# Optimization experiments

Hardware: AMD Instinct MI355X
Metric: run time of the kernel (lower is better)

## Reference

```python
import jax, jax.numpy as jnp
import numpy as np

B, T, CIN, H, W = 1, 8, 32, 256, 256
CO, NH, WS = 64, 8, 8  # C_out, n_head, wind_size


def conv3x3(x, w, b):
    # x: [N, C, h, w], w: [O, I, 3, 3], stride 1, padding 1 (SAME for 3x3)
    y = jax.lax.conv_general_dilated(
        x, w, window_strides=(1, 1), padding=((1, 1), (1, 1)),
        dimension_numbers=("NCHW", "OIHW", "NCHW"))
    return y + b[None, :, None, None]


def setup_inputs() -> dict:
    key = jax.random.key(0)
    ks = jax.random.split(key, 9)
    s = 0.05  # small init scale keeps attention logits well-conditioned
    f32 = jnp.float32
    return {
        "x": jax.random.normal(ks[0], (B, T, CIN, H, W), f32),
        "Wq": jax.random.normal(ks[1], (CO, CIN, 3, 3), f32) * s,
        "bq": jax.random.normal(ks[2], (CO,), f32) * s,
        "Wk": jax.random.normal(ks[3], (CO, CIN, 3, 3), f32) * s,
        "bk": jax.random.normal(ks[4], (CO,), f32) * s,
        "Wv": jax.random.normal(ks[5], (CO, CIN, 3, 3), f32) * s,
        "bv": jax.random.normal(ks[6], (CO,), f32) * s,
        "Wo": jax.random.normal(ks[7], (CO, CO, 3, 3), f32) * s,
        "bo": jax.random.normal(ks[8], (CO,), f32) * s,
    }


def reference(x, Wq, bq, Wk, bk, Wv, bv, Wo, bo):
    b, t, c, h, w = x.shape
    Hg, Wg = h // WS, w // WS          # grid of windows
    hc = CO // NH                      # per-head channels
    d = hc * WS * WS                   # per-window token dim

    # im2grid: [B,T,C,H,W] -> [B*T*Hg*Wg, C, Ws, Ws] (each window a conv batch elem)
    xg = (x.reshape(b, t, c, Hg, WS, Wg, WS)
           .transpose(0, 1, 3, 5, 2, 4, 6)
           .reshape(b * t * Hg * Wg, c, WS, WS))

    def proj(wgt, bias):
        y = conv3x3(xg, wgt, bias)                        # [BTHWg, CO, Ws, Ws]
        y = y.reshape(b, t, Hg * Wg, NH, hc, WS, WS)      # split heads (nh outer in channel)
        return y.transpose(0, 1, 3, 2, 4, 5, 6).reshape(b, t, NH, Hg * Wg, d)

    q, k, v = proj(Wq, bq), proj(Wk, bk), proj(Wv, bv)    # [B,T,nh,HWg,d]

    att = jnp.einsum("btnqd,btnkd->btnqk", q, k) * (1.0 / np.sqrt(d)).astype(x.dtype)
    att = jax.nn.softmax(att, axis=-1)                    # [B,T,nh,HWg,HWg]
    y = jnp.einsum("btnqk,btnkd->btnqd", att, v)          # [B,T,nh,HWg,d]

    # back to image: [B,T,nh,HWg,hc,Ws,Ws] -> [B,T,CO,Hg,Wg,Ws,Ws] -> [B,T,CO,H,W]
    y = (y.reshape(b, t, NH, Hg * Wg, hc, WS, WS)
          .transpose(0, 1, 2, 4, 3, 5, 6)
          .reshape(b, t, CO, Hg, Wg, WS, WS)
          .transpose(0, 1, 2, 3, 5, 4, 6)
          .reshape(b, t, CO, h, w))

    out = y + conv3x3(y.reshape(b * t, CO, h, w), Wo, bo).reshape(b, t, CO, h, w)
    return out
```

## Files before the change

### kernel.cpp

```cpp
#include <hip/hip_runtime.h>
#include <hip/hip_bf16.h>
#include <stdint.h>


using bf16 = __hip_bfloat16;
typedef short bf16x8 __attribute__((ext_vector_type(8)));
typedef float f32x4 __attribute__((ext_vector_type(4)));

#define AS1 __attribute__((address_space(1)))
#define AS3 __attribute__((address_space(3)))

__device__ __forceinline__ void gload_lds16(const void* g, void* l) {
  __builtin_amdgcn_global_load_lds((const AS1 unsigned int*)g, (AS3 unsigned int*)l, 16, 0, 0);
}
__device__ __forceinline__ float b2f(unsigned short u) {
  union { unsigned int i; float f; } x; x.i = ((unsigned)u) << 16; return x.f;
}
__device__ __forceinline__ unsigned short f2b(float f) {
  __hip_bfloat16 h = __float2bfloat16(f);
  return *reinterpret_cast<unsigned short*>(&h);
}

__global__ __launch_bounds__(256) void prep_w(const float* __restrict__ Wq, const float* __restrict__ Wk,
                                              const float* __restrict__ Wv, const float* __restrict__ Wo,
                                              bf16* __restrict__ wt, bf16* __restrict__ wot) {
  int i = blockIdx.x * 256 + threadIdx.x;
  if (i < 9 * 192 * 32) {
    int ci = i & 31, co192 = (i >> 5) % 192, s = i / 6144;
    int dy = s / 3, dx = s % 3;
    int proj = co192 >> 6, co = co192 & 63;
    const float* Ws = (proj == 0) ? Wq : ((proj == 1) ? Wk : Wv);
    wt[i] = __float2bfloat16(Ws[((co * 32 + ci) * 3 + dy) * 3 + dx]);
  }
  if (i < 9 * 64 * 64) {
    int ci = i & 63, co = (i >> 6) & 63, s = i >> 12;
    wot[i] = __float2bfloat16(Wo[((co * 64 + ci) * 3 + (s / 3)) * 3 + (s % 3)]);
  }
}

__global__ __launch_bounds__(256) void qkv_conv(const float* __restrict__ x, const bf16* __restrict__ wt,
                                                const float* __restrict__ bq, const float* __restrict__ bk,
                                                const float* __restrict__ bv,
                                                bf16* __restrict__ qout, bf16* __restrict__ kout,
                                                bf16* __restrict__ vout) {
  __shared__ bf16 smem[192 * 136];
  bf16* xp = smem;
  int tid = threadIdx.x, bid = blockIdx.x;
  int t = bid >> 9, g = bid & 511;
  int gy = g >> 4, gx0 = (g & 15) * 2;

  unsigned int* xp32 = (unsigned int*)xp;
  for (int i = tid; i < 4000; i += 256) xp32[i] = 0u;
  __syncthreads();
  const float* xb = x + (size_t)t * 32 * 65536;
  #pragma unroll
  for (int it = 0; it < 16; ++it) {
    int e = tid + it * 256;
    int ix = e & 7, win = (e >> 3) & 1, iy = (e >> 4) & 7, ci = e >> 7;
    float val = xb[(size_t)ci * 65536 + (gy * 8 + iy) * 256 + (gx0 + win) * 8 + ix];
    xp[(win * 100 + (iy + 1) * 10 + (ix + 1)) * 40 + ci] = __float2bfloat16(val);
  }
  __syncthreads();

  int wv = tid >> 6, l = tid & 63, l15 = l & 15, lg = l >> 4;
  f32x4 z4 = {0.f, 0.f, 0.f, 0.f};
  f32x4 acc[3][8];
  for (int i = 0; i < 3; ++i) for (int j = 0; j < 8; ++j) acc[i][j] = z4;

  #pragma unroll
  for (int s = 0; s < 9; ++s) {
    const int dy = s / 3, dx = s % 3;
    bf16x8 a[3];
    #pragma unroll
    for (int mt = 0; mt < 3; ++mt)
      a[mt] = *(const bf16x8*)&wt[((size_t)s * 192 + wv * 48 + mt * 16 + l15) * 32 + lg * 8];
    #pragma unroll
    for (int nt = 0; nt < 8; ++nt) {
      int n = nt * 16 + l15;
      int win = n >> 6, px = n & 63;
      int iy = px >> 3, ix = px & 7;
      bf16x8 b = *(const bf16x8*)&xp[(win * 100 + (iy + dy) * 10 + (ix + dx)) * 40 + lg * 8];
      #pragma unroll
      for (int mt = 0; mt < 3; ++mt)
        acc[mt][nt] = __builtin_amdgcn_mfma_f32_16x16x32_bf16(a[mt], b, acc[mt][nt], 0, 0, 0);
    }
  }

  __syncthreads();
  bf16* outl = smem;
  #pragma unroll
  for (int mt = 0; mt < 3; ++mt) {
    int c0 = wv * 48 + mt * 16 + lg * 4;
    int proj = c0 >> 6;
    const float* bptr = (proj == 0) ? bq : ((proj == 1) ? bk : bv);
    float bias[4];
    #pragma unroll
    for (int r = 0; r < 4; ++r) bias[r] = bptr[(c0 + r) & 63];
    #pragma unroll
    for (int nt = 0; nt < 8; ++nt) {
      int n = nt * 16 + l15;
      #pragma unroll
      for (int r = 0; r < 4; ++r)
        outl[(c0 + r) * 136 + n] = __float2bfloat16(acc[mt][nt][r] + bias[r]);
    }
  }
  __syncthreads();

  #pragma unroll
  for (int proj = 0; proj < 3; ++proj) {
    bf16* dst = (proj == 0) ? qout : ((proj == 1) ? kout : vout);
    #pragma unroll
    for (int pass = 0; pass < 4; ++pass) {
      int c = pass * 256 + tid;
      int d8 = c & 63, head = (c >> 6) & 7, wn2 = c >> 9;
      int jj = d8 >> 3, px0 = (d8 & 7) * 8;
      bf16x8 val = *(const bf16x8*)&outl[(proj * 64 + head * 8 + jj) * 136 + wn2 * 64 + px0];
      size_t gwin = (size_t)gy * 32 + gx0 + wn2;
      *(bf16x8*)&dst[((size_t)(t * 8 + head) * 1024 + gwin) * 512 + d8 * 8] = val;
    }
  }
}

__global__ __launch_bounds__(256) void transpose_v(const bf16* __restrict__ v, bf16* __restrict__ vt) {
  __shared__ bf16 tl[64 * 72];
  int tid = threadIdx.x, bid = blockIdx.x;
  int bh = bid >> 7, wtile = (bid >> 3) & 15, dtile = bid & 7;
  int w0 = wtile * 64, d0 = dtile * 64;
  const bf16* vb = v + ((size_t)bh * 1024 + w0) * 512 + d0;
  int win_l = tid >> 2, dseg = (tid & 3) * 16;
  bf16x8 x0 = *(const bf16x8*)&vb[(size_t)win_l * 512 + dseg];
  bf16x8 x1 = *(const bf16x8*)&vb[(size_t)win_l * 512 + dseg + 8];
  #pragma unroll
  for (int j = 0; j < 8; ++j) {
    *(short*)&tl[(dseg + j) * 72 + win_l] = x0[j];
    *(short*)&tl[(dseg + 8 + j) * 72 + win_l] = x1[j];
  }
  __syncthreads();
  int d_l = tid >> 2, wseg = (tid & 3) * 16;
  bf16x8 y0 = *(const bf16x8*)&tl[d_l * 72 + wseg];
  bf16x8 y1 = *(const bf16x8*)&tl[d_l * 72 + wseg + 8];
  bf16* vtb = vt + ((size_t)bh * 512 + d_l * 8 + dtile) * 1024 + w0 + wseg;
  *(bf16x8*)&vtb[0] = y0;
  *(bf16x8*)&vtb[8] = y1;
}

__device__ __forceinline__ void stage8(const bf16* __restrict__ Ab, const bf16* __restrict__ Bb,
                                       bf16* smem, int c, int t, int sk,
                                       int w, int lr, int sl) {
  #pragma unroll
  for (int p = 0; p < 4; ++p) {
    int row = p * 64 + w * 8 + lr;
    gload_lds16(Ab + (size_t)row * sk + t * 64 + sl * 8,
                (char*)smem + c * 65536 + p * 8192 + w * 1024);
    gload_lds16(Bb + (size_t)row * sk + t * 64 + sl * 8,
                (char*)smem + c * 65536 + 32768 + p * 8192 + w * 1024);
  }
}

__global__ __launch_bounds__(512, 2) void qk_gemm(const bf16* __restrict__ q, const bf16* __restrict__ k,
                                                  bf16* __restrict__ S) {
  __shared__ bf16 smem[65536];
  int tid = threadIdx.x;
  int bid = (blockIdx.x & 7) * 128 + (blockIdx.x >> 3);
  int batch = bid >> 4, tm = (bid >> 2) & 3, tn = bid & 3;
  const bf16* Qb = q + (size_t)batch * 1024 * 512 + (size_t)tm * 256 * 512;
  const bf16* Kb = k + (size_t)batch * 1024 * 512 + (size_t)tn * 256 * 512;
  int w = tid >> 6, l = tid & 63, l15 = l & 15, lg = l >> 4;
  int wm2 = w >> 2, wn4 = w & 3;
  int lr = l >> 3, sl = (l & 7) ^ lr, swz = l15 & 7;
  f32x4 z4 = {0.f, 0.f, 0.f, 0.f};
  f32x4 acc[8][4];
  for (int i = 0; i < 8; ++i) for (int j = 0; j < 4; ++j) acc[i][j] = z4;

  stage8(Qb, Kb, smem, 0, 0, 512, w, lr, sl);
  asm volatile("s_waitcnt vmcnt(0)" ::: "memory");
  __builtin_amdgcn_s_barrier();
  __builtin_amdgcn_sched_barrier(0);

  for (int t = 0; t < 8; ++t) {
    int c = t & 1;
    if (t + 1 < 8) stage8(Qb, Kb, smem, c ^ 1, t + 1, 512, w, lr, sl);
    const bf16* At = smem + c * 32768;
    const bf16* Bt = At + 16384;
    __builtin_amdgcn_s_setprio(1);
    #pragma unroll
    for (int kk = 0; kk < 2; ++kk) {
      int ps = (kk * 4 + lg) ^ swz;
      bf16x8 a[8], b[4];
      #pragma unroll
      for (int i = 0; i < 8; ++i)
        a[i] = *(const bf16x8*)&At[(wm2 * 128 + i * 16 + l15) * 64 + ps * 8];
      #pragma unroll
      for (int j = 0; j < 4; ++j)
        b[j] = *(const bf16x8*)&Bt[(wn4 * 64 + j * 16 + l15) * 64 + ps * 8];
      #pragma unroll
      for (int i = 0; i < 8; ++i)
        #pragma unroll
        for (int j = 0; j < 4; ++j)
          acc[i][j] = __builtin_amdgcn_mfma_f32_16x16x32_bf16(a[i], b[j], acc[i][j], 0, 0, 0);
    }
    __builtin_amdgcn_s_setprio(0);
    asm volatile("s_waitcnt vmcnt(0)" ::: "memory");
    __builtin_amdgcn_s_barrier();
    __builtin_amdgcn_sched_barrier(0);
  }

  const float SCALE = 0.04419417382415922f;
  bf16* Sb = S + (size_t)batch * 1024 * 1024;
  #pragma unroll
  for (int i = 0; i < 8; ++i)
    #pragma unroll
    for (int j = 0; j < 4; ++j)
      #pragma unroll
      for (int r = 0; r < 4; ++r) {
        int row = tm * 256 + wm2 * 128 + i * 16 + lg * 4 + r;
        int col = tn * 256 + wn4 * 64 + j * 16 + l15;
        Sb[(size_t)row * 1024 + col] = __float2bfloat16(acc[i][j][r] * SCALE);
      }
}

__global__ __launch_bounds__(256) void row_stats(const bf16* __restrict__ S, float2* __restrict__ pstats) {
  int l = threadIdx.x & 63;
  size_t row = (size_t)blockIdx.x * 4 + (threadIdx.x >> 6);
  const bf16* p = S + row * 1024 + l * 16;
  bf16x8 s0 = *(const bf16x8*)p;
  bf16x8 s1 = *(const bf16x8*)(p + 8);
  float f[16];
  #pragma unroll
  for (int i = 0; i < 8; ++i) { f[i] = b2f((unsigned short)s0[i]); f[8 + i] = b2f((unsigned short)s1[i]); }
  float m = f[0];
  #pragma unroll
  for (int i = 1; i < 16; ++i) m = fmaxf(m, f[i]);
  for (int d = 1; d < 64; d <<= 1) m = fmaxf(m, __shfl_xor(m, d));
  float sum = 0.f;
  #pragma unroll
  for (int i = 0; i < 16; ++i) sum += __expf(f[i] - m);
  for (int d = 1; d < 64; d <<= 1) sum += __shfl_xor(sum, d);
  if (l == 0) {
    float2 st; st.x = m; st.y = 1.0f / sum;
    pstats[row] = st;
  }
}

__global__ __launch_bounds__(512, 2) void pv_gemm(const bf16* __restrict__ S, const bf16* __restrict__ vt,
                                                  const float2* __restrict__ pstats,
                                                  bf16* __restrict__ y) {
  __shared__ bf16 smem[65536];
  int tid = threadIdx.x;
  int bid = (blockIdx.x & 7) * 64 + (blockIdx.x >> 3);
  int batch = bid >> 3, bq = (bid >> 1) & 3, bd = bid & 1;
  const bf16* Pb = S + (size_t)batch * 1024 * 1024 + (size_t)bq * 256 * 1024;
  const bf16* Vb = vt + (size_t)batch * 512 * 1024 + (size_t)bd * 256 * 1024;
  int w = tid >> 6, l = tid & 63, l15 = l & 15, lg = l >> 4;
  int wm2 = w >> 2, wn4 = w & 3;
  int lr = l >> 3, sl = (l & 7) ^ lr, swz = l15 & 7;
  f32x4 z4 = {0.f, 0.f, 0.f, 0.f};
  f32x4 acc[8][4];
  for (int i = 0; i < 8; ++i) for (int j = 0; j < 4; ++j) acc[i][j] = z4;

  float m4[4], r4[4];
  #pragma unroll
  for (int p = 0; p < 4; ++p) {
    float2 st = pstats[(size_t)batch * 1024 + bq * 256 + p * 64 + w * 8 + lr];
    m4[p] = st.x; r4[p] = st.y;
  }

  bf16x8 areg[4];
  #define PV_ISSUE(tt, cc)                                                        \
    {                                                                             \
      _Pragma("unroll")                                                           \
      for (int p = 0; p < 4; ++p)                                                 \
        areg[p] = *(const bf16x8*)&Pb[(size_t)(p * 64 + w * 8 + lr) * 1024 +      \
                                      (tt) * 64 + sl * 8];                        \
      _Pragma("unroll")                                                           \
      for (int p = 0; p < 4; ++p)                                                 \
        gload_lds16(Vb + (size_t)(p * 64 + w * 8 + lr) * 1024 + (tt) * 64 + sl * 8, \
                    (char*)smem + (cc) * 65536 + 32768 + p * 8192 + w * 1024);    \
    }
  #define PV_WRITE_A(cc)                                                          \
    {                                                                             \
      _Pragma("unroll")                                                           \
      for (int p = 0; p < 4; ++p) {                                               \
        bf16x8 o;                                                                 \
        _Pragma("unroll")                                                         \
        for (int e = 0; e < 8; ++e) {                                             \
          float fv = b2f((unsigned short)areg[p][e]);                             \
          o[e] = (short)f2b(__expf(fv - m4[p]) * r4[p]);                          \
        }                                                                         \
        *(bf16x8*)((char*)smem + (cc) * 65536 + p * 8192 + w * 1024 + l * 16) = o; \
      }                                                                           \
    }

  PV_ISSUE(0, 0);
  asm volatile("s_waitcnt vmcnt(0)" ::: "memory");
  PV_WRITE_A(0);
  asm volatile("s_waitcnt lgkmcnt(0)" ::: "memory");
  __builtin_amdgcn_s_barrier();
  __builtin_amdgcn_sched_barrier(0);

  for (int t = 0; t < 16; ++t) {
    int c = t & 1;
    if (t + 1 < 16) PV_ISSUE(t + 1, c ^ 1);
    const bf16* At = smem + c * 32768;
    const bf16* Bt = At + 16384;
    __builtin_amdgcn_s_setprio(1);
    #pragma unroll
    for (int kk = 0; kk < 2; ++kk) {
      int ps = (kk * 4 + lg) ^ swz;
      bf16x8 a[8], b[4];
      #pragma unroll
      for (int i = 0; i < 8; ++i)
        a[i] = *(const bf16x8*)&At[(wm2 * 128 + i * 16 + l15) * 64 + ps * 8];
      #pragma unroll
      for (int j = 0; j < 4; ++j)
        b[j] = *(const bf16x8*)&Bt[(wn4 * 64 + j * 16 + l15) * 64 + ps * 8];
      #pragma unroll
      for (int i = 0; i < 8; ++i)
        #pragma unroll
        for (int j = 0; j < 4; ++j)
          acc[i][j] = __builtin_amdgcn_mfma_f32_16x16x32_bf16(a[i], b[j], acc[i][j], 0, 0, 0);
    }
    __builtin_amdgcn_s_setprio(0);
    asm volatile("s_waitcnt vmcnt(0)" ::: "memory");
    if (t + 1 < 16) PV_WRITE_A(c ^ 1);
    asm volatile("s_waitcnt lgkmcnt(0)" ::: "memory");
    __builtin_amdgcn_s_barrier();
    __builtin_amdgcn_sched_barrier(0);
  }

  int t2 = batch >> 3, h = batch & 7;
  #pragma unroll
  for (int i = 0; i < 8; ++i)
    #pragma unroll
    for (int j = 0; j < 4; ++j)
      #pragma unroll
      for (int r = 0; r < 4; ++r) {
        int win = bq * 256 + wm2 * 128 + i * 16 + lg * 4 + r;
        int dp = bd * 256 + wn4 * 64 + j * 16 + l15;
        int jj = dp & 7, pyix = dp >> 3;
        int gy = win >> 5, gx = win & 31;
        int Y = gy * 8 + (pyix >> 3), X = gx * 8 + (pyix & 7);
        y[(((size_t)t2 * 256 + Y) * 256 + X) * 64 + h * 8 + jj] = __float2bfloat16(acc[i][j][r]);
      }
}

__global__ __launch_bounds__(256) void out_conv(const bf16* __restrict__ yimg, const bf16* __restrict__ wot,
                                                const float* __restrict__ bo, float* __restrict__ out) {
  __shared__ bf16 yp[324 * 76];
  int tid = threadIdx.x, bid = blockIdx.x;
  int t = bid >> 8, tile = bid & 255;
  int y0 = (tile >> 4) * 16, x0 = (tile & 15) * 16;
  const bf16* yb = yimg + (size_t)t * 256 * 256 * 64;

  for (int e = tid; e < 324 * 8; e += 256) {
    int seg = e & 7, pos = e >> 3;
    int ppx = pos % 18, ppy = pos / 18;
    int gy = y0 + ppy - 1, gx = x0 + ppx - 1;
    bf16x8 val = {0, 0, 0, 0, 0, 0, 0, 0};
    if ((unsigned)gy < 256u && (unsigned)gx < 256u)
      val = *(const bf16x8*)&yb[((size_t)gy * 256 + gx) * 64 + seg * 8];
    *(bf16x8*)&yp[pos * 76 + seg * 8] = val;
  }
  __syncthreads();

  int wv = tid >> 6, l = tid & 63, l15 = l & 15, lg = l >> 4;
  int wm = wv & 1, wn = wv >> 1;
  f32x4 z4 = {0.f, 0.f, 0.f, 0.f};
  f32x4 acc[2][8];
  for (int i = 0; i < 2; ++i) for (int j = 0; j < 8; ++j) acc[i][j] = z4;

  #pragma unroll
  for (int s9 = 0; s9 < 9; ++s9) {
    const int dy = s9 / 3, dx = s9 % 3;
    #pragma unroll
    for (int half = 0; half < 2; ++half) {
      bf16x8 a[2];
      #pragma unroll
      for (int mt = 0; mt < 2; ++mt)
        a[mt] = *(const bf16x8*)&wot[((size_t)s9 * 64 + wm * 32 + mt * 16 + l15) * 64 + half * 32 + lg * 8];
      #pragma unroll
      for (int nt = 0; nt < 8; ++nt) {
        int ty = wn * 8 + nt;
        bf16x8 b = *(const bf16x8*)&yp[((ty + dy) * 18 + l15 + dx) * 76 + half * 32 + lg * 8];
        #pragma unroll
        for (int mt = 0; mt < 2; ++mt)
          acc[mt][nt] = __builtin_amdgcn_mfma_f32_16x16x32_bf16(a[mt], b, acc[mt][nt], 0, 0, 0);
      }
    }
  }

  float* ob = out + (size_t)t * 64 * 65536;
  float bias[2][4];
  #pragma unroll
  for (int mt = 0; mt < 2; ++mt)
    #pragma unroll
    for (int r = 0; r < 4; ++r) bias[mt][r] = bo[wm * 32 + mt * 16 + lg * 4 + r];
  #pragma unroll
  for (int mt = 0; mt < 2; ++mt)
    #pragma unroll
    for (int nt = 0; nt < 8; ++nt) {
      int ty = wn * 8 + nt;
      #pragma unroll
      for (int r = 0; r < 4; ++r) {
        int co = wm * 32 + mt * 16 + lg * 4 + r;
        float res = b2f(*(const unsigned short*)&yp[((ty + 1) * 18 + l15 + 1) * 76 + co]);
        ob[(size_t)co * 65536 + (size_t)(y0 + ty) * 256 + x0 + l15] = res + acc[mt][nt][r] + bias[mt][r];
      }
    }
}

extern "C" void kernel_launch(void* const* d_in, const int* in_sizes, int n_in,
                              void* d_out, int out_size, void* d_ws, size_t ws_size,
                              hipStream_t stream) {
  const float* x  = (const float*)d_in[0];
  const float* Wq = (const float*)d_in[1];
  const float* bq = (const float*)d_in[2];
  const float* Wk = (const float*)d_in[3];
  const float* bk = (const float*)d_in[4];
  const float* Wv = (const float*)d_in[5];
  const float* bv = (const float*)d_in[6];
  const float* Wo = (const float*)d_in[7];
  const float* bo = (const float*)d_in[8];
  float* out = (float*)d_out;

  char* ws = (char*)d_ws;
  bf16* wt  = (bf16*)(ws + 0);
  bf16* wot = (bf16*)(ws + 110592);
  bf16* q   = (bf16*)(ws + 262144);
  bf16* k   = (bf16*)(ws + 67371008);
  float2* pstats = (float2*)(ws + 67371008);
  bf16* v   = (bf16*)(ws + 134479872);
  bf16* S   = (bf16*)(ws + 134479872);
  bf16* vt  = (bf16*)(ws + 268697600);
  bf16* y   = (bf16*)(ws + 262144);

  prep_w<<<216, 256, 0, stream>>>(Wq, Wk, Wv, Wo, wt, wot);
  qkv_conv<<<4096, 256, 0, stream>>>(x, wt, bq, bk, bv, q, k, v);
  transpose_v<<<8192, 256, 0, stream>>>(v, vt);
  qk_gemm<<<1024, 512, 0, stream>>>(q, k, S);
  row_stats<<<16384, 256, 0, stream>>>(S, pstats);
  pv_gemm<<<512, 512, 0, stream>>>(S, vt, pstats, y);
  out_conv<<<2048, 256, 0, stream>>>(y, wot, bo, out);
}
```

Measured before the change: 442.1 us.

## Fuse softmax row statistics into QK GEMM epilogue and halve QKV staging LDS

The QK GEMM epilogue now computes per-tile row max and sum-of-exp from the fp32 accumulators and writes them as partial stats. A small combine kernel merges them, replacing the row_stats pass that re-read the whole bf16 score matrix. The QKV conv now stages its output through LDS in two halves, which halves its shared-memory footprint so more blocks can be resident, and its global stores become wider contiguous runs. The fused path runs only if the workspace is large enough for the partial-stats buffer, and the stats now come from fp32 values rather than the bf16-rounded scores.

```diff
diff --git a/kernel.cpp b/kernel.cpp
--- a/kernel.cpp
+++ b/kernel.cpp
@@ -43,7 +43,7 @@
                                                 const float* __restrict__ bv,
                                                 bf16* __restrict__ qout, bf16* __restrict__ kout,
                                                 bf16* __restrict__ vout) {
-  __shared__ bf16 smem[192 * 136];
+  __shared__ bf16 smem[13056];
   bf16* xp = smem;
   int tid = threadIdx.x, bid = blockIdx.x;
   int t = bid >> 9, g = bid & 511;
@@ -89,35 +89,44 @@
   __syncthreads();
   bf16* outl = smem;
   #pragma unroll
-  for (int mt = 0; mt < 3; ++mt) {
-    int c0 = wv * 48 + mt * 16 + lg * 4;
-    int proj = c0 >> 6;
-    const float* bptr = (proj == 0) ? bq : ((proj == 1) ? bk : bv);
-    float bias[4];
-    #pragma unroll
-    for (int r = 0; r < 4; ++r) bias[r] = bptr[(c0 + r) & 63];
-    #pragma unroll
-    for (int nt = 0; nt < 8; ++nt) {
-      int n = nt * 16 + l15;
-      #pragma unroll
-      for (int r = 0; r < 4; ++r)
-        outl[(c0 + r) * 136 + n] = __float2bfloat16(acc[mt][nt][r] + bias[r]);
-    }
-  }
-  __syncthreads();
-
-  #pragma unroll
-  for (int proj = 0; proj < 3; ++proj) {
-    bf16* dst = (proj == 0) ? qout : ((proj == 1) ? kout : vout);
-    #pragma unroll
-    for (int pass = 0; pass < 4; ++pass) {
-      int c = pass * 256 + tid;
-      int d8 = c & 63, head = (c >> 6) & 7, wn2 = c >> 9;
-      int jj = d8 >> 3, px0 = (d8 & 7) * 8;
-      bf16x8 val = *(const bf16x8*)&outl[(proj * 64 + head * 8 + jj) * 136 + wn2 * 64 + px0];
-      size_t gwin = (size_t)gy * 32 + gx0 + wn2;
-      *(bf16x8*)&dst[((size_t)(t * 8 + head) * 1024 + gwin) * 512 + d8 * 8] = val;
-    }
+  for (int half = 0; half < 2; ++half) {
+    if ((wv >> 1) == half) {
+      #pragma unroll
+      for (int mt = 0; mt < 3; ++mt) {
+        int c0 = wv * 48 + mt * 16 + lg * 4;
+        int rl0 = c0 - half * 96;
+        int proj = c0 >> 6;
+        const float* bptr = (proj == 0) ? bq : ((proj == 1) ? bk : bv);
+        float bias[4];
+        #pragma unroll
+        for (int r = 0; r < 4; ++r) bias[r] = bptr[(c0 + r) & 63];
+        #pragma unroll
+        for (int nt = 0; nt < 8; ++nt) {
+          int n = nt * 16 + l15;
+          #pragma unroll
+          for (int r = 0; r < 4; ++r)
+            outl[(rl0 + r) * 136 + n] = __float2bfloat16(acc[mt][nt][r] + bias[r]);
+        }
+      }
+    }
+    __syncthreads();
+    #pragma unroll
+    for (int it = 0; it < 3; ++it) {
+      int c = it * 256 + tid;
+      int row_l = c >> 3, ch = c & 7;
+      int grow = half * 96 + row_l;
+      int proj = grow >> 6, head = (grow >> 3) & 7, jj = grow & 7;
+      int win2 = ch >> 2, px0 = (ch & 3) * 16;
+      const bf16* src = &outl[row_l * 136 + win2 * 64 + px0];
+      bf16x8 v0 = *(const bf16x8*)src;
+      bf16x8 v1 = *(const bf16x8*)(src + 8);
+      bf16* dstp = (proj == 0) ? qout : ((proj == 1) ? kout : vout);
+      size_t gwin = (size_t)gy * 32 + gx0 + win2;
+      bf16* d = &dstp[((size_t)(t * 8 + head) * 1024 + gwin) * 512 + jj * 64 + px0];
+      *(bf16x8*)d = v0;
+      *(bf16x8*)(d + 8) = v1;
+    }
+    if (half == 0) __syncthreads();
   }
 }
 
@@ -158,7 +167,7 @@
 }
 
 __global__ __launch_bounds__(512, 2) void qk_gemm(const bf16* __restrict__ q, const bf16* __restrict__ k,
-                                                  bf16* __restrict__ S) {
+                                                  bf16* __restrict__ S, float2* __restrict__ part) {
   __shared__ bf16 smem[65536];
   int tid = threadIdx.x;
   int bid = (blockIdx.x & 7) * 128 + (blockIdx.x >> 3);
@@ -217,6 +226,44 @@
         int col = tn * 256 + wn4 * 64 + j * 16 + l15;
         Sb[(size_t)row * 1024 + col] = __float2bfloat16(acc[i][j][r] * SCALE);
       }
+
+  if (part != nullptr) {
+    #pragma unroll
+    for (int i = 0; i < 8; ++i)
+      #pragma unroll
+      for (int r = 0; r < 4; ++r) {
+        float v0 = acc[i][0][r] * SCALE, v1 = acc[i][1][r] * SCALE;
+        float v2 = acc[i][2][r] * SCALE, v3 = acc[i][3][r] * SCALE;
+        float m = fmaxf(fmaxf(v0, v1), fmaxf(v2, v3));
+        #pragma unroll
+        for (int d = 1; d < 16; d <<= 1) m = fmaxf(m, __shfl_xor(m, d));
+        float s = __expf(v0 - m) + __expf(v1 - m) + __expf(v2 - m) + __expf(v3 - m);
+        #pragma unroll
+        for (int d = 1; d < 16; d <<= 1) s += __shfl_xor(s, d);
+        if (l15 == 0) {
+          int grow = tm * 256 + wm2 * 128 + i * 16 + lg * 4 + r;
+          float2 st; st.x = m; st.y = s;
+          part[((size_t)batch * 1024 + grow) * 16 + tn * 4 + wn4] = st;
+        }
+      }
+  }
+}
+
+__global__ __launch_bounds__(256) void combine_stats(const float2* __restrict__ part,
+                                                     float2* __restrict__ pstats) {
+  int row = blockIdx.x * 256 + threadIdx.x;
+  const float2* p = part + (size_t)row * 16;
+  float2 v[16];
+  #pragma unroll
+  for (int i = 0; i < 16; ++i) v[i] = p[i];
+  float m = v[0].x;
+  #pragma unroll
+  for (int i = 1; i < 16; ++i) m = fmaxf(m, v[i].x);
+  float s = 0.f;
+  #pragma unroll
+  for (int i = 0; i < 16; ++i) s += v[i].y * __expf(v[i].x - m);
+  float2 st; st.x = m; st.y = 1.0f / s;
+  pstats[row] = st;
 }
 
 __global__ __launch_bounds__(256) void row_stats(const bf16* __restrict__ S, float2* __restrict__ pstats) {
@@ -429,16 +476,23 @@
   bf16* q   = (bf16*)(ws + 262144);
   bf16* k   = (bf16*)(ws + 67371008);
   float2* pstats = (float2*)(ws + 67371008);
-  bf16* v   = (bf16*)(ws + 134479872);
   bf16* S   = (bf16*)(ws + 134479872);
   bf16* vt  = (bf16*)(ws + 268697600);
   bf16* y   = (bf16*)(ws + 262144);
+  bf16* v   = S;
+  const size_t PART_OFF = 335806464ull;
+  const size_t PART_BYTES = 64ull * 1024 * 16 * sizeof(float2);
+  bool fused_stats = (ws_size >= PART_OFF + PART_BYTES);
+  float2* part = fused_stats ? (float2*)(ws + PART_OFF) : nullptr;
 
   prep_w<<<216, 256, 0, stream>>>(Wq, Wk, Wv, Wo, wt, wot);
   qkv_conv<<<4096, 256, 0, stream>>>(x, wt, bq, bk, bv, q, k, v);
   transpose_v<<<8192, 256, 0, stream>>>(v, vt);
-  qk_gemm<<<1024, 512, 0, stream>>>(q, k, S);
-  row_stats<<<16384, 256, 0, stream>>>(S, pstats);
+  qk_gemm<<<1024, 512, 0, stream>>>(q, k, S, part);
+  if (fused_stats)
+    combine_stats<<<256, 256, 0, stream>>>(part, pstats);
+  else
+    row_stats<<<16384, 256, 0, stream>>>(S, pstats);
   pv_gemm<<<512, 512, 0, stream>>>(S, vt, pstats, y);
   out_conv<<<2048, 256, 0, stream>>>(y, wot, bo, out);
 }
```

After: 481.4 us. +8.9%, slower.

## Deepen qk_gemm into a 4-stage LDS ring with three tiles in flight

Applied to the files above, without the earlier changes.

Replaces the double-buffered K=64 staging in qk_gemm with a 4-slot ring of K=32 tiles that keeps three global-to-LDS loads in flight. Waits use partial vmcnt counts, so each iteration only blocks on the oldest tile, with one barrier per step. The LDS swizzle is adapted to the narrower 32-element rows. The aim is to hide global load latency behind MFMA work, at the cost of twice as many iterations and barriers with less MFMA work between them. The v pointer is now written as an alias of S, but it is the same address as before.

```diff
diff --git a/kernel.cpp b/kernel.cpp
--- a/kernel.cpp
+++ b/kernel.cpp
@@ -144,19 +144,6 @@
   *(bf16x8*)&vtb[8] = y1;
 }
 
-__device__ __forceinline__ void stage8(const bf16* __restrict__ Ab, const bf16* __restrict__ Bb,
-                                       bf16* smem, int c, int t, int sk,
-                                       int w, int lr, int sl) {
-  #pragma unroll
-  for (int p = 0; p < 4; ++p) {
-    int row = p * 64 + w * 8 + lr;
-    gload_lds16(Ab + (size_t)row * sk + t * 64 + sl * 8,
-                (char*)smem + c * 65536 + p * 8192 + w * 1024);
-    gload_lds16(Bb + (size_t)row * sk + t * 64 + sl * 8,
-                (char*)smem + c * 65536 + 32768 + p * 8192 + w * 1024);
-  }
-}
-
 __global__ __launch_bounds__(512, 2) void qk_gemm(const bf16* __restrict__ q, const bf16* __restrict__ k,
                                                   bf16* __restrict__ S) {
   __shared__ bf16 smem[65536];
@@ -167,43 +154,58 @@
   const bf16* Kb = k + (size_t)batch * 1024 * 512 + (size_t)tn * 256 * 512;
   int w = tid >> 6, l = tid & 63, l15 = l & 15, lg = l >> 4;
   int wm2 = w >> 2, wn4 = w & 3;
-  int lr = l >> 3, sl = (l & 7) ^ lr, swz = l15 & 7;
+  int srow_lo = l >> 2;
+  int ssl = (l & 3) ^ (srow_lo & 3);
+  int swz2 = l15 & 3;
   f32x4 z4 = {0.f, 0.f, 0.f, 0.f};
   f32x4 acc[8][4];
   for (int i = 0; i < 8; ++i) for (int j = 0; j < 4; ++j) acc[i][j] = z4;
 
-  stage8(Qb, Kb, smem, 0, 0, 512, w, lr, sl);
-  asm volatile("s_waitcnt vmcnt(0)" ::: "memory");
-  __builtin_amdgcn_s_barrier();
-  __builtin_amdgcn_sched_barrier(0);
-
-  for (int t = 0; t < 8; ++t) {
-    int c = t & 1;
-    if (t + 1 < 8) stage8(Qb, Kb, smem, c ^ 1, t + 1, 512, w, lr, sl);
-    const bf16* At = smem + c * 32768;
-    const bf16* Bt = At + 16384;
-    __builtin_amdgcn_s_setprio(1);
-    #pragma unroll
-    for (int kk = 0; kk < 2; ++kk) {
-      int ps = (kk * 4 + lg) ^ swz;
-      bf16x8 a[8], b[4];
-      #pragma unroll
-      for (int i = 0; i < 8; ++i)
-        a[i] = *(const bf16x8*)&At[(wm2 * 128 + i * 16 + l15) * 64 + ps * 8];
-      #pragma unroll
-      for (int j = 0; j < 4; ++j)
-        b[j] = *(const bf16x8*)&Bt[(wn4 * 64 + j * 16 + l15) * 64 + ps * 8];
-      #pragma unroll
-      for (int i = 0; i < 8; ++i)
-        #pragma unroll
-        for (int j = 0; j < 4; ++j)
-          acc[i][j] = __builtin_amdgcn_mfma_f32_16x16x32_bf16(a[i], b[j], acc[i][j], 0, 0, 0);
-    }
-    __builtin_amdgcn_s_setprio(0);
-    asm volatile("s_waitcnt vmcnt(0)" ::: "memory");
+  #define QK_STAGE(T)                                                            \
+    {                                                                            \
+      char* sbase = (char*)smem + ((T) & 3) * 32768;                             \
+      _Pragma("unroll")                                                          \
+      for (int p = 0; p < 2; ++p) {                                              \
+        int row = p * 128 + w * 16 + srow_lo;                                    \
+        gload_lds16(Qb + (size_t)row * 512 + (T) * 32 + ssl * 8,                 \
+                    sbase + p * 8192 + w * 1024);                                \
+        gload_lds16(Kb + (size_t)row * 512 + (T) * 32 + ssl * 8,                 \
+                    sbase + 16384 + p * 8192 + w * 1024);                        \
+      }                                                                          \
+    }
+
+  QK_STAGE(0); QK_STAGE(1); QK_STAGE(2);
+
+  #pragma unroll
+  for (int t = 0; t < 16; ++t) {
+    if (t <= 13)      asm volatile("s_waitcnt vmcnt(8)" ::: "memory");
+    else if (t == 14) asm volatile("s_waitcnt vmcnt(4)" ::: "memory");
+    else              asm volatile("s_waitcnt vmcnt(0)" ::: "memory");
     __builtin_amdgcn_s_barrier();
     __builtin_amdgcn_sched_barrier(0);
-  }
+
+    const int se = (t & 3) * 16384;
+    bf16x8 a[8], b[4];
+    #pragma unroll
+    for (int i = 0; i < 8; ++i)
+      a[i] = *(const bf16x8*)&smem[se + (wm2 * 128 + i * 16 + l15) * 32 + ((lg ^ swz2) * 8)];
+    #pragma unroll
+    for (int j = 0; j < 4; ++j)
+      b[j] = *(const bf16x8*)&smem[se + 8192 + (wn4 * 64 + j * 16 + l15) * 32 + ((lg ^ swz2) * 8)];
+
+    if (t <= 12) QK_STAGE(t + 3);
+
+    asm volatile("s_waitcnt lgkmcnt(0)" ::: "memory");
+    __builtin_amdgcn_sched_barrier(0);
+    __builtin_amdgcn_s_setprio(1);
+    #pragma unroll
+    for (int i = 0; i < 8; ++i)
+      #pragma unroll
+      for (int j = 0; j < 4; ++j)
+        acc[i][j] = __builtin_amdgcn_mfma_f32_16x16x32_bf16(a[i], b[j], acc[i][j], 0, 0, 0);
+    __builtin_amdgcn_s_setprio(0);
+  }
+  #undef QK_STAGE
 
   const float SCALE = 0.04419417382415922f;
   bf16* Sb = S + (size_t)batch * 1024 * 1024;
@@ -429,10 +431,10 @@
   bf16* q   = (bf16*)(ws + 262144);
   bf16* k   = (bf16*)(ws + 67371008);
   float2* pstats = (float2*)(ws + 67371008);
-  bf16* v   = (bf16*)(ws + 134479872);
   bf16* S   = (bf16*)(ws + 134479872);
   bf16* vt  = (bf16*)(ws + 268697600);
   bf16* y   = (bf16*)(ws + 262144);
+  bf16* v   = S;
 
   prep_w<<<216, 256, 0, stream>>>(Wq, Wk, Wv, Wo, wt, wot);
   qkv_conv<<<4096, 256, 0, stream>>>(x, wt, bq, bk, bv, q, k, v);
```

Result: no change. 450.0 us (+1.8%).

## Permute QKV feature order to drop LDS staging in qkv_conv epilogue

Applied to the files above, without the earlier changes.

The qkv_conv epilogue now writes bias-added accumulators straight to global memory as 4-element packs, skipping the LDS output staging and its two barriers. To make this possible, the per-window feature dimension is reordered from channel-major to pixel-major, and transpose_v's output indexing is changed to match. This is valid because the attention dot products and PV products are invariant to a consistent permutation of d. The shared-memory footprint of qkv_conv shrinks, which may allow more resident blocks, and out_conv gets a min-blocks occupancy hint. The trade-off is narrower, more scattered 8-byte global stores, and the change depends on pv_gemm's output mapping staying consistent with the new layout.

```diff
diff --git a/kernel.cpp b/kernel.cpp
--- a/kernel.cpp
+++ b/kernel.cpp
@@ -5,6 +5,7 @@
 
 using bf16 = __hip_bfloat16;
 typedef short bf16x8 __attribute__((ext_vector_type(8)));
+typedef short bf16x4 __attribute__((ext_vector_type(4)));
 typedef float f32x4 __attribute__((ext_vector_type(4)));
 
 #define AS1 __attribute__((address_space(1)))
@@ -43,8 +44,7 @@
                                                 const float* __restrict__ bv,
                                                 bf16* __restrict__ qout, bf16* __restrict__ kout,
                                                 bf16* __restrict__ vout) {
-  __shared__ bf16 smem[192 * 136];
-  bf16* xp = smem;
+  __shared__ bf16 xp[8000];
   int tid = threadIdx.x, bid = blockIdx.x;
   int t = bid >> 9, g = bid & 511;
   int gy = g >> 4, gx0 = (g & 15) * 2;
@@ -86,37 +86,27 @@
     }
   }
 
-  __syncthreads();
-  bf16* outl = smem;
   #pragma unroll
   for (int mt = 0; mt < 3; ++mt) {
     int c0 = wv * 48 + mt * 16 + lg * 4;
     int proj = c0 >> 6;
+    int co0 = c0 & 63;
+    int head = co0 >> 3, jj0 = co0 & 7;
     const float* bptr = (proj == 0) ? bq : ((proj == 1) ? bk : bv);
+    bf16* dst = (proj == 0) ? qout : ((proj == 1) ? kout : vout);
     float bias[4];
     #pragma unroll
-    for (int r = 0; r < 4; ++r) bias[r] = bptr[(c0 + r) & 63];
+    for (int r = 0; r < 4; ++r) bias[r] = bptr[co0 + r];
+    size_t bh = (size_t)(t * 8 + head);
     #pragma unroll
     for (int nt = 0; nt < 8; ++nt) {
       int n = nt * 16 + l15;
-      #pragma unroll
-      for (int r = 0; r < 4; ++r)
-        outl[(c0 + r) * 136 + n] = __float2bfloat16(acc[mt][nt][r] + bias[r]);
-    }
-  }
-  __syncthreads();
-
-  #pragma unroll
-  for (int proj = 0; proj < 3; ++proj) {
-    bf16* dst = (proj == 0) ? qout : ((proj == 1) ? kout : vout);
-    #pragma unroll
-    for (int pass = 0; pass < 4; ++pass) {
-      int c = pass * 256 + tid;
-      int d8 = c & 63, head = (c >> 6) & 7, wn2 = c >> 9;
-      int jj = d8 >> 3, px0 = (d8 & 7) * 8;
-      bf16x8 val = *(const bf16x8*)&outl[(proj * 64 + head * 8 + jj) * 136 + wn2 * 64 + px0];
-      size_t gwin = (size_t)gy * 32 + gx0 + wn2;
-      *(bf16x8*)&dst[((size_t)(t * 8 + head) * 1024 + gwin) * 512 + d8 * 8] = val;
+      int win2 = n >> 6, pyix = n & 63;
+      size_t gwin = (size_t)gy * 32 + gx0 + win2;
+      bf16x4 pack;
+      #pragma unroll
+      for (int r = 0; r < 4; ++r) pack[r] = (short)f2b(acc[mt][nt][r] + bias[r]);
+      *(bf16x4*)&dst[(bh * 1024 + gwin) * 512 + pyix * 8 + jj0] = pack;
     }
   }
 }
@@ -139,7 +129,7 @@
   int d_l = tid >> 2, wseg = (tid & 3) * 16;
   bf16x8 y0 = *(const bf16x8*)&tl[d_l * 72 + wseg];
   bf16x8 y1 = *(const bf16x8*)&tl[d_l * 72 + wseg + 8];
-  bf16* vtb = vt + ((size_t)bh * 512 + d_l * 8 + dtile) * 1024 + w0 + wseg;
+  bf16* vtb = vt + ((size_t)bh * 512 + d0 + d_l) * 1024 + w0 + wseg;
   *(bf16x8*)&vtb[0] = y0;
   *(bf16x8*)&vtb[8] = y1;
 }
@@ -344,8 +334,8 @@
       }
 }
 
-__global__ __launch_bounds__(256) void out_conv(const bf16* __restrict__ yimg, const bf16* __restrict__ wot,
-                                                const float* __restrict__ bo, float* __restrict__ out) {
+__global__ __launch_bounds__(256, 4) void out_conv(const bf16* __restrict__ yimg, const bf16* __restrict__ wot,
+                                                   const float* __restrict__ bo, float* __restrict__ out) {
   __shared__ bf16 yp[324 * 76];
   int tid = threadIdx.x, bid = blockIdx.x;
   int t = bid >> 8, tile = bid & 255;
@@ -429,10 +419,10 @@
   bf16* q   = (bf16*)(ws + 262144);
   bf16* k   = (bf16*)(ws + 67371008);
   float2* pstats = (float2*)(ws + 67371008);
-  bf16* v   = (bf16*)(ws + 134479872);
   bf16* S   = (bf16*)(ws + 134479872);
   bf16* vt  = (bf16*)(ws + 268697600);
   bf16* y   = (bf16*)(ws + 262144);
+  bf16* v   = S;
 
   prep_w<<<216, 256, 0, stream>>>(Wq, Wk, Wv, Wo, wt, wot);
   qkv_conv<<<4096, 256, 0, stream>>>(x, wt, bq, bk, bv, q, k, v);
```

Measured after the change: 434.8 us. No clear change (-1.7%).
